# Optimization experiments

Measured on AMD Instinct MI355X. Metric: run time of the kernel, lower is better.

## Reference

```python
import jax, jax.numpy as jnp
import numpy as np

EPS = 1e-7
N_NODES = 100000

# --- Lorentz model (c = 1), working at the origin o = (1, 0, ..., 0) ---

def expmap0(v_spatial):
    """Exp map at origin: tangent spatial part [N, d] -> hyperboloid point [N, d+1]."""
    nrm = jnp.sqrt(jnp.maximum(jnp.sum(v_spatial * v_spatial, axis=-1, keepdims=True), EPS))
    x0 = jnp.cosh(nrm)
    xs = jnp.sinh(nrm) / nrm * v_spatial
    return jnp.concatenate([x0, xs], axis=-1)


def logmap0(x):
    """Log map at origin: point [N, d+1] -> tangent spatial part [N, d]."""
    x0 = jnp.maximum(x[..., :1], 1.0 + EPS)
    xs = x[..., 1:]
    nrm = jnp.sqrt(jnp.maximum(jnp.sum(xs * xs, axis=-1, keepdims=True), EPS))
    return jnp.arccosh(x0) / nrm * xs


def sigmoid_nonlin(x):
    # log map -> sigmoid in tangent space -> exp map (c_in = c_out = 1)
    return expmap0(jax.nn.sigmoid(logmap0(x)))


def hgcn_layer(x, edge_index, W, b):
    """HGCN conv: tangent-space linear + mean aggregation over edges + exp map."""
    t = logmap0(x)                      # [N, d_in]
    h = t @ W + b                       # [N, d_out]
    src, dst = edge_index[0], edge_index[1]
    msg = h[src]                        # [E, d_out] gather
    agg = jax.ops.segment_sum(msg, dst, num_segments=N_NODES)
    deg = jax.ops.segment_sum(jnp.ones((edge_index.shape[1],), h.dtype), dst,
                              num_segments=N_NODES)
    agg = agg / jnp.maximum(deg, 1.0)[:, None]
    return expmap0(agg)


def setup_inputs() -> dict:
    key = jax.random.key(0)
    ks = jax.random.split(key, 10)
    d_in, h1, h2, h_mlp, d_out = 64, 64, 64, 128, 40
    return {
        "features": jax.random.normal(ks[0], (N_NODES, d_in), jnp.float32),
        "edge_index": jax.random.randint(ks[1], (2, 1600000), 0, N_NODES, jnp.int64),
        "W1": jax.random.normal(ks[2], (d_in, h1), jnp.float32) * 0.05,
        "b1": jnp.zeros((h1,), jnp.float32),
        "W2": jax.random.normal(ks[3], (h1, h2), jnp.float32) * 0.05,
        "b2": jnp.zeros((h2,), jnp.float32),
        "W3": jax.random.normal(ks[4], (h2, h_mlp), jnp.float32) * 0.05,
        "b3": jnp.zeros((h_mlp,), jnp.float32),
        "W4": jax.random.normal(ks[5], (h_mlp, d_out), jnp.float32) * 0.05,
        "b4": jnp.zeros((d_out,), jnp.float32),
    }


def reference(features, edge_index, W1, b1, W2, b2, W3, b3, W4, b4):
    # lift Euclidean features to the hyperboloid (pad time coord, exp map)
    x = expmap0(features)                       # [N, d_in+1]
    x = hgcn_layer(x, edge_index, W1, b1)
    x = sigmoid_nonlin(x)
    x = hgcn_layer(x, edge_index, W2, b2)
    x = sigmoid_nonlin(x)
    t = logmap0(x)                              # [N, h2] (spatial part, drops time coord)
    # MLP head (dropout inactive at eval)
    h = jax.nn.relu(t @ W3 + b3)
    return h @ W4 + b4
```

## Files before the change

kernel.cpp:

```cpp
#include <hip/hip_runtime.h>


constexpr int CSHIFT = 8;
constexpr int CNODES = 1 << CSHIFT;
constexpr int EPB    = 4096;
constexpr int PTHR   = 512;
constexpr int EPT    = EPB / PTHR;
constexpr int CAP    = 6144;

constexpr int W1F_OFF = 0;
constexpr int W2F_OFF = 4096;
constexpr int W3F_OFF = 8192;
constexpr int W4F_OFF = 16384;
constexpr int WIMG_TOT = 22528;

typedef __attribute__((ext_vector_type(8))) short short8;
typedef __attribute__((ext_vector_type(4))) float floatx4;

__device__ __forceinline__ float sigmoidf(float x) {
    return 1.0f / (1.0f + __expf(-x));
}
__device__ __forceinline__ unsigned short f2bf(float f) {
    unsigned int u = __float_as_uint(f);
    u = (u + 0x7FFFu + ((u >> 16) & 1u)) >> 16;
    return (unsigned short)u;
}

__global__ __launch_bounds__(512) void part_prep_k(
    const int* __restrict__ src, const int* __restrict__ dst,
    int* __restrict__ ccur, int* __restrict__ arena, int E, int NBUCK, int gP,
    const float* __restrict__ feat, unsigned short* __restrict__ featbf,
    const float* __restrict__ W1, const float* __restrict__ W2,
    const float* __restrict__ W3, const float* __restrict__ W4,
    unsigned short* __restrict__ img, int n8)
{
    __shared__ int  hist[512];
    __shared__ int  exoff[512];
    __shared__ int  lcur[512];
    __shared__ int  gbase[512];
    __shared__ int  wsum[8];
    __shared__ int  stage[EPB];
    __shared__ unsigned short stageS[EPB];

    const int tid = threadIdx.x;

    if ((int)blockIdx.x >= gP) {
        int i = ((int)blockIdx.x - gP) * PTHR + tid;
        if (i < n8) {
            const float4* p = (const float4*)feat + (size_t)i * 2;
            float4 a = p[0], b = p[1];
            uint4 o;
            o.x = (unsigned)f2bf(a.x) | ((unsigned)f2bf(a.y) << 16);
            o.y = (unsigned)f2bf(a.z) | ((unsigned)f2bf(a.w) << 16);
            o.z = (unsigned)f2bf(b.x) | ((unsigned)f2bf(b.y) << 16);
            o.w = (unsigned)f2bf(b.z) | ((unsigned)f2bf(b.w) << 16);
            ((uint4*)featbf)[i] = o;
            return;
        }
        int t = i - n8;
        if (t >= WIMG_TOT) return;
        float v = 0.f;
        int s = t;
        if (s < W2F_OFF) {
            int j = s & 7, m = (s >> 3) & 15, q = (s >> 7) & 3, kk = (s >> 9) & 1, c = s >> 10;
            v = W1[(kk * 32 + q * 8 + j) * 64 + c * 16 + m];
        } else if (s < W3F_OFF) {
            s -= W2F_OFF;
            int j = s & 7, m = (s >> 3) & 15, q = (s >> 7) & 3, kk = (s >> 9) & 1, c = s >> 10;
            v = W2[(kk * 32 + q * 8 + j) * 64 + c * 16 + m];
        } else if (s < W4F_OFF) {
            s -= W3F_OFF;
            int j = s & 7, m = (s >> 3) & 15, q = (s >> 7) & 3, kk = (s >> 9) & 1, c = s >> 10;
            v = W3[(kk * 32 + q * 8 + j) * 128 + c * 16 + m];
        } else {
            s -= W4F_OFF;
            int j = s & 7, m = (s >> 3) & 15, q = (s >> 7) & 3, kk = (s >> 9) & 3, c = s >> 11;
            int n = c * 16 + m;
            if (n < 40) v = W4[(kk * 32 + q * 8 + j) * 40 + n];
        }
        img[t] = f2bf(v);
        return;
    }

    const int e0  = blockIdx.x * EPB;
    const int ec  = min(EPB, E - e0);
    const int lane = tid & 63, wid = tid >> 6;

    int pk[EPT], bk[EPT];
    hist[tid] = 0;
    __syncthreads();
    #pragma unroll
    for (int j = 0; j < EPT; j++) {
        int idx = tid + j * PTHR;
        if (idx < ec) {
            int s = src[e0 + idx];
            int d = dst[e0 + idx];
            bk[j] = d >> CSHIFT;
            pk[j] = s | ((d & (CNODES - 1)) << 17);
            atomicAdd(&hist[bk[j]], 1);
        } else bk[j] = -1;
    }
    __syncthreads();
    int h = hist[tid];
    int v = h;
    #pragma unroll
    for (int d = 1; d < 64; d <<= 1) {
        int t = __shfl_up(v, d);
        if (lane >= d) v += t;
    }
    if (lane == 63) wsum[wid] = v;
    __syncthreads();
    if (tid == 0) {
        int s = 0;
        #pragma unroll
        for (int k = 0; k < 8; k++) { int t = wsum[k]; wsum[k] = s; s += t; }
    }
    __syncthreads();
    {
        int ex = wsum[wid] + v - h;
        int gb = 0;
        if (tid < NBUCK && h > 0) gb = atomicAdd(ccur + tid, h);
        exoff[tid] = ex;
        lcur[tid]  = ex;
        gbase[tid] = gb;
    }
    __syncthreads();
    #pragma unroll
    for (int j = 0; j < EPT; j++) {
        if (bk[j] >= 0) {
            int l = atomicAdd(&lcur[bk[j]], 1);
            stage[l]  = pk[j];
            stageS[l] = (unsigned short)bk[j];
        }
    }
    __syncthreads();
    for (int i = tid; i < ec; i += PTHR) {
        int b = stageS[i];
        arena[(size_t)b * CAP + gbase[b] + (i - exoff[b])] = stage[i];
    }
}

__global__ __launch_bounds__(1024) void csr_fine(const int* __restrict__ arena,
                                                 const int* __restrict__ ccur,
                                                 int* __restrict__ off,
                                                 int* __restrict__ ssrc,
                                                 int N, int E, int NBUCK) {
    __shared__ int part[512];
    __shared__ int cnt[CNODES];
    __shared__ int cur[CNODES];
    __shared__ int wpre[8];
    __shared__ int wpre2[4];
    const int b = blockIdx.x;
    const int node0 = b << CSHIFT;
    const int tid = threadIdx.x;
    const int lane = tid & 63, wid = tid >> 6;

    int c0 = 0, v0 = 0;
    if (tid < 512) {
        c0 = (tid < NBUCK) ? ccur[tid] : 0;
        v0 = c0;
        #pragma unroll
        for (int d = 1; d < 64; d <<= 1) {
            int t = __shfl_up(v0, d);
            if (lane >= d) v0 += t;
        }
        if (lane == 63) wpre[wid] = v0;
    }
    __syncthreads();
    if (tid == 0) {
        int s = 0;
        #pragma unroll
        for (int k = 0; k < 8; k++) { int t = wpre[k]; wpre[k] = s; s += t; }
    }
    __syncthreads();
    if (tid < 512) part[tid] = wpre[wid] + v0;
    __syncthreads();
    const int cbeg = (b > 0) ? part[b - 1] : 0;
    const int ec   = min(ccur[b], CAP);
    if (b == 0 && tid == 0) off[N] = E;

    if (tid < CNODES) cnt[tid] = 0;
    __syncthreads();
    const int* pe = arena + (size_t)b * CAP;
    for (int i = tid; i < ec; i += 1024)
        atomicAdd(&cnt[(pe[i] >> 17) & (CNODES - 1)], 1);
    __syncthreads();

    int c = 0, v = 0;
    if (tid < CNODES) {
        c = cnt[tid];
        v = c;
        #pragma unroll
        for (int d = 1; d < 64; d <<= 1) {
            int t = __shfl_up(v, d);
            if (lane >= d) v += t;
        }
        if (lane == 63) wpre2[wid] = v;
    }
    __syncthreads();
    if (tid == 0) {
        int s = 0;
        #pragma unroll
        for (int k = 0; k < CNODES / 64; k++) { int t = wpre2[k]; wpre2[k] = s; s += t; }
    }
    __syncthreads();
    if (tid < CNODES) {
        int ex = wpre2[wid] + v - c;
        cur[tid] = ex;
        int node = node0 + tid;
        if (node < N) off[node] = cbeg + ex;
    }
    __syncthreads();
    for (int i = tid; i < ec; i += 1024) {
        int p = pe[i];
        int pos = cbeg + atomicAdd(&cur[(p >> 17) & (CNODES - 1)], 1);
        ssrc[pos] = p & 0x1FFFF;
    }
}

#define ACC8(v)                                    \
    acc[0] += __uint_as_float((v).x << 16);        \
    acc[1] += __uint_as_float((v).x & 0xFFFF0000u);\
    acc[2] += __uint_as_float((v).y << 16);        \
    acc[3] += __uint_as_float((v).y & 0xFFFF0000u);\
    acc[4] += __uint_as_float((v).z << 16);        \
    acc[5] += __uint_as_float((v).z & 0xFFFF0000u);\
    acc[6] += __uint_as_float((v).w << 16);        \
    acc[7] += __uint_as_float((v).w & 0xFFFF0000u);

__device__ __forceinline__ void gather_tile_wave(
    const unsigned short* __restrict__ h, const int* __restrict__ off,
    const int* __restrict__ ssrc, unsigned short* Agg, int rowB, int N,
    int w, int lane)
{
    #pragma unroll
    for (int pass = 0; pass < 2; pass++) {
        int rl = w * 16 + pass * 8 + (lane >> 3);
        int g  = rowB + rl;
        int q  = (lane & 7) * 8;
        uint4 p = make_uint4(0u, 0u, 0u, 0u);
        if (g < N) {
            int beg = off[g], end = off[g + 1];
            float acc[8] = {0.f, 0.f, 0.f, 0.f, 0.f, 0.f, 0.f, 0.f};
            int i = beg;
            for (; i + 8 <= end; i += 8) {
                uint4 v0 = *(const uint4*)(h + (size_t)ssrc[i]     * 64 + q);
                uint4 v1 = *(const uint4*)(h + (size_t)ssrc[i + 1] * 64 + q);
                uint4 v2 = *(const uint4*)(h + (size_t)ssrc[i + 2] * 64 + q);
                uint4 v3 = *(const uint4*)(h + (size_t)ssrc[i + 3] * 64 + q);
                uint4 v4 = *(const uint4*)(h + (size_t)ssrc[i + 4] * 64 + q);
                uint4 v5 = *(const uint4*)(h + (size_t)ssrc[i + 5] * 64 + q);
                uint4 v6 = *(const uint4*)(h + (size_t)ssrc[i + 6] * 64 + q);
                uint4 v7 = *(const uint4*)(h + (size_t)ssrc[i + 7] * 64 + q);
                ACC8(v0); ACC8(v1); ACC8(v2); ACC8(v3);
                ACC8(v4); ACC8(v5); ACC8(v6); ACC8(v7);
            }
            for (; i + 2 <= end; i += 2) {
                uint4 v0 = *(const uint4*)(h + (size_t)ssrc[i]     * 64 + q);
                uint4 v1 = *(const uint4*)(h + (size_t)ssrc[i + 1] * 64 + q);
                ACC8(v0); ACC8(v1);
            }
            for (; i < end; i++) {
                uint4 v = *(const uint4*)(h + (size_t)ssrc[i] * 64 + q);
                ACC8(v);
            }
            float inv = __builtin_amdgcn_rcpf((float)max(end - beg, 1));
            p.x = (unsigned)f2bf(acc[0]*inv) | ((unsigned)f2bf(acc[1]*inv) << 16);
            p.y = (unsigned)f2bf(acc[2]*inv) | ((unsigned)f2bf(acc[3]*inv) << 16);
            p.z = (unsigned)f2bf(acc[4]*inv) | ((unsigned)f2bf(acc[5]*inv) << 16);
            p.w = (unsigned)f2bf(acc[6]*inv) | ((unsigned)f2bf(acc[7]*inv) << 16);
        }
        *(uint4*)(Agg + rl * 72 + q) = p;
    }
}

__global__ __launch_bounds__(128) void aggemm1_k(
    const unsigned short* __restrict__ featbf, const int* __restrict__ off,
    const int* __restrict__ ssrc, const unsigned short* __restrict__ img,
    const float* __restrict__ bias, unsigned short* __restrict__ t1, int N)
{
    __shared__ alignas(16) unsigned short Agg[32 * 72];

    const int tid = threadIdx.x;
    const int rowB = blockIdx.x * 32;
    const int w = tid >> 6, lane = tid & 63;
    const int m = lane & 15, quad = lane >> 4;
    const int row0 = rowB + w * 16;

    gather_tile_wave(featbf, off, ssrc, Agg, rowB, N, w, lane);

    const short8* Wf = (const short8*)(img + W1F_OFF);
    floatx4 acc[4];
    #pragma unroll
    for (int c = 0; c < 4; c++) acc[c] = (floatx4){0.f, 0.f, 0.f, 0.f};
    #pragma unroll
    for (int kk = 0; kk < 2; kk++) {
        short8 a = *(const short8*)(Agg + (w * 16 + m) * 72 + kk * 32 + quad * 8);
        #pragma unroll
        for (int c = 0; c < 4; c++) {
            short8 b = Wf[((c * 2 + kk) * 4 + quad) * 16 + m];
            acc[c] = __builtin_amdgcn_mfma_f32_16x16x32_bf16(a, b, acc[c], 0, 0, 0);
        }
    }
    bool dzr[4];
    int rows[4];
    #pragma unroll
    for (int r = 0; r < 4; r++) {
        rows[r] = row0 + quad * 4 + r;
        dzr[r] = (rows[r] < N) ? (off[rows[r] + 1] == off[rows[r]]) : false;
    }
    #pragma unroll
    for (int c = 0; c < 4; c++) {
        int col = c * 16 + m;
        float bv = bias[col];
        #pragma unroll
        for (int r = 0; r < 4; r++) {
            if (rows[r] < N) {
                float v = dzr[r] ? 0.5f : sigmoidf(acc[c][r] + bv);
                t1[(size_t)rows[r] * 64 + col] = f2bf(v);
            }
        }
    }
}

__global__ __launch_bounds__(128) void aggep3_k(
    const unsigned short* __restrict__ t1, const int* __restrict__ off,
    const int* __restrict__ ssrc, const unsigned short* __restrict__ img,
    const float* __restrict__ b2, const float* __restrict__ b3,
    const float* __restrict__ b4, float* __restrict__ out, int N)
{
    __shared__ alignas(16) unsigned short SM[4608];
    unsigned short* T2  = SM;
    unsigned short* Agg = SM + 2304;
    unsigned short* H3h = SM + 2304;

    const int tid = threadIdx.x;
    const int rowB = blockIdx.x * 32;
    const int w = tid >> 6, lane = tid & 63;
    const int m = lane & 15, quad = lane >> 4;
    const int row0 = rowB + w * 16;

    gather_tile_wave(t1, off, ssrc, Agg, rowB, N, w, lane);

    {
        const short8* Wf = (const short8*)(img + W2F_OFF);
        floatx4 acc[4];
        #pragma unroll
        for (int c = 0; c < 4; c++) acc[c] = (floatx4){0.f, 0.f, 0.f, 0.f};
        #pragma unroll
        for (int kk = 0; kk < 2; kk++) {
            short8 a = *(const short8*)(Agg + (w * 16 + m) * 72 + kk * 32 + quad * 8);
            #pragma unroll
            for (int c = 0; c < 4; c++) {
                short8 b = Wf[((c * 2 + kk) * 4 + quad) * 16 + m];
                acc[c] = __builtin_amdgcn_mfma_f32_16x16x32_bf16(a, b, acc[c], 0, 0, 0);
            }
        }
        bool dzr[4];
        #pragma unroll
        for (int r = 0; r < 4; r++) {
            int row = row0 + quad * 4 + r;
            dzr[r] = (row < N) ? (off[row + 1] == off[row]) : false;
        }
        #pragma unroll
        for (int c = 0; c < 4; c++) {
            int col = c * 16 + m;
            float bv = b2[col];
            #pragma unroll
            for (int r = 0; r < 4; r++) {
                int rl = w * 16 + quad * 4 + r;
                float v = dzr[r] ? 0.5f : sigmoidf(acc[c][r] + bv);
                T2[rl * 72 + col] = f2bf(v);
            }
        }
    }

    floatx4 acc2[3];
    #pragma unroll
    for (int c = 0; c < 3; c++) acc2[c] = (floatx4){0.f, 0.f, 0.f, 0.f};
    const short8* Wf3 = (const short8*)(img + W3F_OFF);
    const short8* Wf4 = (const short8*)(img + W4F_OFF);

    #pragma unroll
    for (int half = 0; half < 2; half++) {
        floatx4 acc[4];
        #pragma unroll
        for (int c = 0; c < 4; c++) acc[c] = (floatx4){0.f, 0.f, 0.f, 0.f};
        #pragma unroll
        for (int kk = 0; kk < 2; kk++) {
            short8 a = *(const short8*)(T2 + (w * 16 + m) * 72 + kk * 32 + quad * 8);
            #pragma unroll
            for (int c = 0; c < 4; c++) {
                short8 b = Wf3[(((half * 4 + c) * 2 + kk) * 4 + quad) * 16 + m];
                acc[c] = __builtin_amdgcn_mfma_f32_16x16x32_bf16(a, b, acc[c], 0, 0, 0);
            }
        }
        #pragma unroll
        for (int c = 0; c < 4; c++) {
            int col = c * 16 + m;
            float bv = b3[half * 64 + col];
            #pragma unroll
            for (int r = 0; r < 4; r++) {
                int rl = w * 16 + quad * 4 + r;
                H3h[rl * 72 + col] = f2bf(fmaxf(acc[c][r] + bv, 0.f));
            }
        }
        #pragma unroll
        for (int kk2 = 0; kk2 < 2; kk2++) {
            short8 a = *(const short8*)(H3h + (w * 16 + m) * 72 + kk2 * 32 + quad * 8);
            #pragma unroll
            for (int c = 0; c < 3; c++) {
                short8 b = Wf4[((c * 4 + half * 2 + kk2) * 4 + quad) * 16 + m];
                acc2[c] = __builtin_amdgcn_mfma_f32_16x16x32_bf16(a, b, acc2[c], 0, 0, 0);
            }
        }
    }

    #pragma unroll
    for (int c = 0; c < 3; c++) {
        int col = c * 16 + m;
        if (col < 40) {
            float bv = b4[col];
            #pragma unroll
            for (int r = 0; r < 4; r++) {
                int row = row0 + quad * 4 + r;
                if (row < N) out[(size_t)row * 40 + col] = acc2[c][r] + bv;
            }
        }
    }
}

extern "C" void kernel_launch(void* const* d_in, const int* in_sizes, int n_in,
                              void* d_out, int out_size, void* d_ws, size_t ws_size,
                              hipStream_t stream)
{
    const float* feat = (const float*)d_in[0];
    const int*   eidx = (const int*)d_in[1];
    const float* W1 = (const float*)d_in[2];
    const float* b1 = (const float*)d_in[3];
    const float* W2 = (const float*)d_in[4];
    const float* b2 = (const float*)d_in[5];
    const float* W3 = (const float*)d_in[6];
    const float* b3 = (const float*)d_in[7];
    const float* W4 = (const float*)d_in[8];
    const float* b4 = (const float*)d_in[9];

    const int N = in_sizes[0] / 64;
    const int E = in_sizes[1] / 2;
    const int* src = eidx;
    const int* dst = eidx + E;

    const int NBUCK = (N + CNODES - 1) / CNODES;

    unsigned short* featbf = (unsigned short*)d_ws;
    unsigned short* t1     = featbf + (size_t)N * 64;
    unsigned short* img    = t1     + (size_t)N * 64;
    int*   off   = (int*)(img + WIMG_TOT);
    int*   ccur  = off + (N + 1);
    int*   ssrc  = ccur + NBUCK;
    int*   arena = ssrc + E;
    float* out   = (float*)d_out;

    hipMemsetAsync(ccur, 0, (size_t)NBUCK * sizeof(int), stream);

    const int gP  = (E + EPB - 1) / EPB;
    const int g32 = (N + 31) / 32;
    const int n8  = N * 64 / 8;
    const int gPC = (n8 + WIMG_TOT + PTHR - 1) / PTHR;

    part_prep_k<<<gP + gPC, dim3(PTHR), 0, stream>>>(src, dst, ccur, arena, E,
                                                     NBUCK, gP, feat, featbf,
                                                     W1, W2, W3, W4, img, n8);
    csr_fine<<<NBUCK, dim3(1024), 0, stream>>>(arena, ccur, off, ssrc, N, E, NBUCK);

    aggemm1_k<<<g32, dim3(128), 0, stream>>>(featbf, off, ssrc, img, b1, t1, N);
    aggep3_k<<<g32, dim3(128), 0, stream>>>(t1, off, ssrc, img, b2, b3, b4, out, N);
}
```

Before: 211.7 us.

## Sort CSR neighbors by source sub-range and enlarge gather blocks to 128 rows

The fine CSR build now buckets each destination node's edges into 8 sub-bins by source index high bits, so the neighbor lists are ordered by source region and the offset array becomes 8 entries per node. The intent is better cache locality for the feature gathers. The aggregation kernels also move from 32-row, 128-thread blocks to 128-row, 512-thread blocks with correspondingly larger shared memory. This costs an 8x larger offset array, more shared-memory atomics and scan work in csr_fine, and changes occupancy.

```diff
diff --git a/kernel.cpp b/kernel.cpp
--- a/kernel.cpp
+++ b/kernel.cpp
@@ -7,6 +7,8 @@
 constexpr int PTHR   = 512;
 constexpr int EPT    = EPB / PTHR;
 constexpr int CAP    = 6144;
+constexpr int SSH    = 14;
+constexpr int NBIN   = CNODES * 8;
 
 constexpr int W1F_OFF = 0;
 constexpr int W2F_OFF = 4096;
@@ -142,14 +144,14 @@
 
 __global__ __launch_bounds__(1024) void csr_fine(const int* __restrict__ arena,
                                                  const int* __restrict__ ccur,
-                                                 int* __restrict__ off,
+                                                 int* __restrict__ off2,
                                                  int* __restrict__ ssrc,
                                                  int N, int E, int NBUCK) {
     __shared__ int part[512];
-    __shared__ int cnt[CNODES];
-    __shared__ int cur[CNODES];
+    __shared__ int cnt[NBIN];
+    __shared__ int cur[NBIN];
     __shared__ int wpre[8];
-    __shared__ int wpre2[4];
+    __shared__ int wpre2[16];
     const int b = blockIdx.x;
     const int node0 = b << CSHIFT;
     const int tid = threadIdx.x;
@@ -177,43 +179,51 @@
     __syncthreads();
     const int cbeg = (b > 0) ? part[b - 1] : 0;
     const int ec   = min(ccur[b], CAP);
-    if (b == 0 && tid == 0) off[N] = E;
-
-    if (tid < CNODES) cnt[tid] = 0;
+    if (b == 0 && tid == 0) off2[8 * N] = E;
+
+    cnt[tid] = 0;
+    cnt[tid + 1024] = 0;
     __syncthreads();
     const int* pe = arena + (size_t)b * CAP;
-    for (int i = tid; i < ec; i += 1024)
-        atomicAdd(&cnt[(pe[i] >> 17) & (CNODES - 1)], 1);
-    __syncthreads();
-
-    int c = 0, v = 0;
-    if (tid < CNODES) {
-        c = cnt[tid];
-        v = c;
-        #pragma unroll
-        for (int d = 1; d < 64; d <<= 1) {
-            int t = __shfl_up(v, d);
-            if (lane >= d) v += t;
-        }
-        if (lane == 63) wpre2[wid] = v;
-    }
+    for (int i = tid; i < ec; i += 1024) {
+        int p = pe[i];
+        int key = (((p >> 17) & (CNODES - 1)) << 3) | ((p & 0x1FFFF) >> SSH);
+        atomicAdd(&cnt[key], 1);
+    }
+    __syncthreads();
+
+    const int t2 = tid * 2;
+    int s0 = cnt[t2], s1 = cnt[t2 + 1];
+    int tsum = s0 + s1;
+    int v = tsum;
+    #pragma unroll
+    for (int d = 1; d < 64; d <<= 1) {
+        int t = __shfl_up(v, d);
+        if (lane >= d) v += t;
+    }
+    if (lane == 63) wpre2[wid] = v;
     __syncthreads();
     if (tid == 0) {
         int s = 0;
         #pragma unroll
-        for (int k = 0; k < CNODES / 64; k++) { int t = wpre2[k]; wpre2[k] = s; s += t; }
-    }
-    __syncthreads();
-    if (tid < CNODES) {
-        int ex = wpre2[wid] + v - c;
-        cur[tid] = ex;
-        int node = node0 + tid;
-        if (node < N) off[node] = cbeg + ex;
+        for (int k = 0; k < 16; k++) { int t = wpre2[k]; wpre2[k] = s; s += t; }
+    }
+    __syncthreads();
+    const int ex0 = wpre2[wid] + v - tsum;
+    cur[t2]     = ex0;
+    cur[t2 + 1] = ex0 + s0;
+    {
+        int node = node0 + (t2 >> 3);
+        if (node < N) {
+            off2[node0 * 8 + t2]     = cbeg + ex0;
+            off2[node0 * 8 + t2 + 1] = cbeg + ex0 + s0;
+        }
     }
     __syncthreads();
     for (int i = tid; i < ec; i += 1024) {
         int p = pe[i];
-        int pos = cbeg + atomicAdd(&cur[(p >> 17) & (CNODES - 1)], 1);
+        int key = (((p >> 17) & (CNODES - 1)) << 3) | ((p & 0x1FFFF) >> SSH);
+        int pos = cbeg + atomicAdd(&cur[key], 1);
         ssrc[pos] = p & 0x1FFFF;
     }
 }
@@ -229,7 +239,7 @@
     acc[7] += __uint_as_float((v).w & 0xFFFF0000u);
 
 __device__ __forceinline__ void gather_tile_wave(
-    const unsigned short* __restrict__ h, const int* __restrict__ off,
+    const unsigned short* __restrict__ h, const int* __restrict__ off2,
     const int* __restrict__ ssrc, unsigned short* Agg, int rowB, int N,
     int w, int lane)
 {
@@ -240,7 +250,7 @@
         int q  = (lane & 7) * 8;
         uint4 p = make_uint4(0u, 0u, 0u, 0u);
         if (g < N) {
-            int beg = off[g], end = off[g + 1];
+            int beg = off2[g * 8], end = off2[g * 8 + 8];
             float acc[8] = {0.f, 0.f, 0.f, 0.f, 0.f, 0.f, 0.f, 0.f};
             int i = beg;
             for (; i + 8 <= end; i += 8) {
@@ -274,20 +284,20 @@
     }
 }
 
-__global__ __launch_bounds__(128) void aggemm1_k(
-    const unsigned short* __restrict__ featbf, const int* __restrict__ off,
+__global__ __launch_bounds__(512) void aggemm1_k(
+    const unsigned short* __restrict__ featbf, const int* __restrict__ off2,
     const int* __restrict__ ssrc, const unsigned short* __restrict__ img,
     const float* __restrict__ bias, unsigned short* __restrict__ t1, int N)
 {
-    __shared__ alignas(16) unsigned short Agg[32 * 72];
+    __shared__ alignas(16) unsigned short Agg[128 * 72];
 
     const int tid = threadIdx.x;
-    const int rowB = blockIdx.x * 32;
+    const int rowB = blockIdx.x * 128;
     const int w = tid >> 6, lane = tid & 63;
     const int m = lane & 15, quad = lane >> 4;
     const int row0 = rowB + w * 16;
 
-    gather_tile_wave(featbf, off, ssrc, Agg, rowB, N, w, lane);
+    gather_tile_wave(featbf, off2, ssrc, Agg, rowB, N, w, lane);
 
     const short8* Wf = (const short8*)(img + W1F_OFF);
     floatx4 acc[4];
@@ -307,7 +317,7 @@
     #pragma unroll
     for (int r = 0; r < 4; r++) {
         rows[r] = row0 + quad * 4 + r;
-        dzr[r] = (rows[r] < N) ? (off[rows[r] + 1] == off[rows[r]]) : false;
+        dzr[r] = (rows[r] < N) ? (off2[rows[r] * 8 + 8] == off2[rows[r] * 8]) : false;
     }
     #pragma unroll
     for (int c = 0; c < 4; c++) {
@@ -323,24 +333,24 @@
     }
 }
 
-__global__ __launch_bounds__(128) void aggep3_k(
-    const unsigned short* __restrict__ t1, const int* __restrict__ off,
+__global__ __launch_bounds__(512) void aggep3_k(
+    const unsigned short* __restrict__ t1, const int* __restrict__ off2,
     const int* __restrict__ ssrc, const unsigned short* __restrict__ img,
     const float* __restrict__ b2, const float* __restrict__ b3,
     const float* __restrict__ b4, float* __restrict__ out, int N)
 {
-    __shared__ alignas(16) unsigned short SM[4608];
+    __shared__ alignas(16) unsigned short SM[18432];
     unsigned short* T2  = SM;
-    unsigned short* Agg = SM + 2304;
-    unsigned short* H3h = SM + 2304;
+    unsigned short* Agg = SM + 9216;
+    unsigned short* H3h = SM + 9216;
 
     const int tid = threadIdx.x;
-    const int rowB = blockIdx.x * 32;
+    const int rowB = blockIdx.x * 128;
     const int w = tid >> 6, lane = tid & 63;
     const int m = lane & 15, quad = lane >> 4;
     const int row0 = rowB + w * 16;
 
-    gather_tile_wave(t1, off, ssrc, Agg, rowB, N, w, lane);
+    gather_tile_wave(t1, off2, ssrc, Agg, rowB, N, w, lane);
 
     {
         const short8* Wf = (const short8*)(img + W2F_OFF);
@@ -360,7 +370,7 @@
         #pragma unroll
         for (int r = 0; r < 4; r++) {
             int row = row0 + quad * 4 + r;
-            dzr[r] = (row < N) ? (off[row + 1] == off[row]) : false;
+            dzr[r] = (row < N) ? (off2[row * 8 + 8] == off2[row * 8]) : false;
         }
         #pragma unroll
         for (int c = 0; c < 4; c++) {
@@ -455,24 +465,24 @@
     unsigned short* featbf = (unsigned short*)d_ws;
     unsigned short* t1     = featbf + (size_t)N * 64;
     unsigned short* img    = t1     + (size_t)N * 64;
-    int*   off   = (int*)(img + WIMG_TOT);
-    int*   ccur  = off + (N + 1);
+    int*   off2  = (int*)(img + WIMG_TOT);
+    int*   ccur  = off2 + ((size_t)8 * N + 1);
     int*   ssrc  = ccur + NBUCK;
     int*   arena = ssrc + E;
     float* out   = (float*)d_out;
 
     hipMemsetAsync(ccur, 0, (size_t)NBUCK * sizeof(int), stream);
 
-    const int gP  = (E + EPB - 1) / EPB;
-    const int g32 = (N + 31) / 32;
-    const int n8  = N * 64 / 8;
-    const int gPC = (n8 + WIMG_TOT + PTHR - 1) / PTHR;
+    const int gP   = (E + EPB - 1) / EPB;
+    const int g128 = (N + 127) / 128;
+    const int n8   = N * 64 / 8;
+    const int gPC  = (n8 + WIMG_TOT + PTHR - 1) / PTHR;
 
     part_prep_k<<<gP + gPC, dim3(PTHR), 0, stream>>>(src, dst, ccur, arena, E,
                                                      NBUCK, gP, feat, featbf,
                                                      W1, W2, W3, W4, img, n8);
-    csr_fine<<<NBUCK, dim3(1024), 0, stream>>>(arena, ccur, off, ssrc, N, E, NBUCK);
-
-    aggemm1_k<<<g32, dim3(128), 0, stream>>>(featbf, off, ssrc, img, b1, t1, N);
-    aggep3_k<<<g32, dim3(128), 0, stream>>>(t1, off, ssrc, img, b2, b3, b4, out, N);
-}
+    csr_fine<<<NBUCK, dim3(1024), 0, stream>>>(arena, ccur, off2, ssrc, N, E, NBUCK);
+
+    aggemm1_k<<<g128, dim3(512), 0, stream>>>(featbf, off2, ssrc, img, b1, t1, N);
+    aggep3_k<<<g128, dim3(512), 0, stream>>>(t1, off2, ssrc, img, b2, b3, b4, out, N);
+}
```

Measured after the change: 216.7 us. 1.02x slower.

## Merge partition, prep and CSR build into one cooperative kernel with grid syncs

Applied to the files above, without the earlier changes.

Replaces the memset, the partition/prep kernel and the CSR fine-sort kernel with one cooperative kernel that zeroes the bucket counters, partitions edges, converts features and weights, then builds the CSR after grid-wide barriers. The goal is to remove two launches and the memset plus their inter-kernel gaps. In exchange, feature conversion becomes a grid-stride loop over fewer blocks, CSR blocks now run with 512 threads instead of 1024, and grid.sync adds barrier cost. The cooperative launch also requires every block to be co-resident.

```diff
diff --git a/kernel.cpp b/kernel.cpp
--- a/kernel.cpp
+++ b/kernel.cpp
@@ -1,4 +1,7 @@
 #include <hip/hip_runtime.h>
+#include <hip/hip_cooperative_groups.h>
+
+namespace cg = cooperative_groups;
 
 
 constexpr int CSHIFT = 8;
@@ -26,14 +29,18 @@
     return (unsigned short)u;
 }
 
-__global__ __launch_bounds__(512) void part_prep_k(
+__global__ __launch_bounds__(PTHR) void prep_all_k(
     const int* __restrict__ src, const int* __restrict__ dst,
-    int* __restrict__ ccur, int* __restrict__ arena, int E, int NBUCK, int gP,
+    int* __restrict__ ccur, int* __restrict__ arena,
+    int* __restrict__ off, int* __restrict__ ssrc,
+    int E, int N, int NBUCK, int gP,
     const float* __restrict__ feat, unsigned short* __restrict__ featbf,
     const float* __restrict__ W1, const float* __restrict__ W2,
     const float* __restrict__ W3, const float* __restrict__ W4,
     unsigned short* __restrict__ img, int n8)
 {
+    cg::grid_group grid = cg::this_grid();
+
     __shared__ int  hist[512];
     __shared__ int  exoff[512];
     __shared__ int  lcur[512];
@@ -41,180 +48,177 @@
     __shared__ int  wsum[8];
     __shared__ int  stage[EPB];
     __shared__ unsigned short stageS[EPB];
+    __shared__ int  cnt[CNODES];
+    __shared__ int  cur[CNODES];
+    __shared__ int  wpre2[4];
+    __shared__ int  cbeg_s;
 
     const int tid = threadIdx.x;
-
-    if ((int)blockIdx.x >= gP) {
-        int i = ((int)blockIdx.x - gP) * PTHR + tid;
-        if (i < n8) {
-            const float4* p = (const float4*)feat + (size_t)i * 2;
-            float4 a = p[0], b = p[1];
-            uint4 o;
-            o.x = (unsigned)f2bf(a.x) | ((unsigned)f2bf(a.y) << 16);
-            o.y = (unsigned)f2bf(a.z) | ((unsigned)f2bf(a.w) << 16);
-            o.z = (unsigned)f2bf(b.x) | ((unsigned)f2bf(b.y) << 16);
-            o.w = (unsigned)f2bf(b.z) | ((unsigned)f2bf(b.w) << 16);
-            ((uint4*)featbf)[i] = o;
-            return;
-        }
-        int t = i - n8;
-        if (t >= WIMG_TOT) return;
-        float v = 0.f;
-        int s = t;
-        if (s < W2F_OFF) {
-            int j = s & 7, m = (s >> 3) & 15, q = (s >> 7) & 3, kk = (s >> 9) & 1, c = s >> 10;
-            v = W1[(kk * 32 + q * 8 + j) * 64 + c * 16 + m];
-        } else if (s < W3F_OFF) {
-            s -= W2F_OFF;
-            int j = s & 7, m = (s >> 3) & 15, q = (s >> 7) & 3, kk = (s >> 9) & 1, c = s >> 10;
-            v = W2[(kk * 32 + q * 8 + j) * 64 + c * 16 + m];
-        } else if (s < W4F_OFF) {
-            s -= W3F_OFF;
-            int j = s & 7, m = (s >> 3) & 15, q = (s >> 7) & 3, kk = (s >> 9) & 1, c = s >> 10;
-            v = W3[(kk * 32 + q * 8 + j) * 128 + c * 16 + m];
-        } else {
-            s -= W4F_OFF;
-            int j = s & 7, m = (s >> 3) & 15, q = (s >> 7) & 3, kk = (s >> 9) & 3, c = s >> 11;
-            int n = c * 16 + m;
-            if (n < 40) v = W4[(kk * 32 + q * 8 + j) * 40 + n];
-        }
-        img[t] = f2bf(v);
-        return;
-    }
-
-    const int e0  = blockIdx.x * EPB;
-    const int ec  = min(EPB, E - e0);
+    const int bid = blockIdx.x;
     const int lane = tid & 63, wid = tid >> 6;
 
-    int pk[EPT], bk[EPT];
-    hist[tid] = 0;
-    __syncthreads();
-    #pragma unroll
-    for (int j = 0; j < EPT; j++) {
-        int idx = tid + j * PTHR;
-        if (idx < ec) {
-            int s = src[e0 + idx];
-            int d = dst[e0 + idx];
-            bk[j] = d >> CSHIFT;
-            pk[j] = s | ((d & (CNODES - 1)) << 17);
-            atomicAdd(&hist[bk[j]], 1);
-        } else bk[j] = -1;
-    }
-    __syncthreads();
-    int h = hist[tid];
-    int v = h;
-    #pragma unroll
-    for (int d = 1; d < 64; d <<= 1) {
-        int t = __shfl_up(v, d);
-        if (lane >= d) v += t;
-    }
-    if (lane == 63) wsum[wid] = v;
-    __syncthreads();
-    if (tid == 0) {
-        int s = 0;
-        #pragma unroll
-        for (int k = 0; k < 8; k++) { int t = wsum[k]; wsum[k] = s; s += t; }
-    }
-    __syncthreads();
+    if (bid == 0 && tid < NBUCK) ccur[tid] = 0;
+    __threadfence();
+    grid.sync();
+
+    if (bid < gP) {
+        const int e0 = bid * EPB;
+        const int ec = min(EPB, E - e0);
+
+        int pk[EPT], bk[EPT];
+        hist[tid] = 0;
+        __syncthreads();
+        #pragma unroll
+        for (int j = 0; j < EPT; j++) {
+            int idx = tid + j * PTHR;
+            if (idx < ec) {
+                int s = src[e0 + idx];
+                int d = dst[e0 + idx];
+                bk[j] = d >> CSHIFT;
+                pk[j] = s | ((d & (CNODES - 1)) << 17);
+                atomicAdd(&hist[bk[j]], 1);
+            } else bk[j] = -1;
+        }
+        __syncthreads();
+        int h = hist[tid];
+        int v = h;
+        #pragma unroll
+        for (int d = 1; d < 64; d <<= 1) {
+            int t = __shfl_up(v, d);
+            if (lane >= d) v += t;
+        }
+        if (lane == 63) wsum[wid] = v;
+        __syncthreads();
+        if (tid == 0) {
+            int s = 0;
+            #pragma unroll
+            for (int k = 0; k < 8; k++) { int t = wsum[k]; wsum[k] = s; s += t; }
+        }
+        __syncthreads();
+        {
+            int ex = wsum[wid] + v - h;
+            int gb = 0;
+            if (tid < NBUCK && h > 0) gb = atomicAdd(ccur + tid, h);
+            exoff[tid] = ex;
+            lcur[tid]  = ex;
+            gbase[tid] = gb;
+        }
+        __syncthreads();
+        #pragma unroll
+        for (int j = 0; j < EPT; j++) {
+            if (bk[j] >= 0) {
+                int l = atomicAdd(&lcur[bk[j]], 1);
+                stage[l]  = pk[j];
+                stageS[l] = (unsigned short)bk[j];
+            }
+        }
+        __syncthreads();
+        for (int i = tid; i < ec; i += PTHR) {
+            int b = stageS[i];
+            arena[(size_t)b * CAP + gbase[b] + (i - exoff[b])] = stage[i];
+        }
+    }
+
     {
-        int ex = wsum[wid] + v - h;
-        int gb = 0;
-        if (tid < NBUCK && h > 0) gb = atomicAdd(ccur + tid, h);
-        exoff[tid] = ex;
-        lcur[tid]  = ex;
-        gbase[tid] = gb;
-    }
-    __syncthreads();
-    #pragma unroll
-    for (int j = 0; j < EPT; j++) {
-        if (bk[j] >= 0) {
-            int l = atomicAdd(&lcur[bk[j]], 1);
-            stage[l]  = pk[j];
-            stageS[l] = (unsigned short)bk[j];
-        }
-    }
-    __syncthreads();
-    for (int i = tid; i < ec; i += PTHR) {
-        int b = stageS[i];
-        arena[(size_t)b * CAP + gbase[b] + (i - exoff[b])] = stage[i];
-    }
-}
-
-__global__ __launch_bounds__(1024) void csr_fine(const int* __restrict__ arena,
-                                                 const int* __restrict__ ccur,
-                                                 int* __restrict__ off,
-                                                 int* __restrict__ ssrc,
-                                                 int N, int E, int NBUCK) {
-    __shared__ int part[512];
-    __shared__ int cnt[CNODES];
-    __shared__ int cur[CNODES];
-    __shared__ int wpre[8];
-    __shared__ int wpre2[4];
-    const int b = blockIdx.x;
-    const int node0 = b << CSHIFT;
-    const int tid = threadIdx.x;
-    const int lane = tid & 63, wid = tid >> 6;
-
-    int c0 = 0, v0 = 0;
-    if (tid < 512) {
-        c0 = (tid < NBUCK) ? ccur[tid] : 0;
-        v0 = c0;
+        const int nW = n8 + WIMG_TOT;
+        for (int i = bid * PTHR + tid; i < nW; i += gridDim.x * PTHR) {
+            if (i < n8) {
+                const float4* p = (const float4*)feat + (size_t)i * 2;
+                float4 a = p[0], b = p[1];
+                uint4 o;
+                o.x = (unsigned)f2bf(a.x) | ((unsigned)f2bf(a.y) << 16);
+                o.y = (unsigned)f2bf(a.z) | ((unsigned)f2bf(a.w) << 16);
+                o.z = (unsigned)f2bf(b.x) | ((unsigned)f2bf(b.y) << 16);
+                o.w = (unsigned)f2bf(b.z) | ((unsigned)f2bf(b.w) << 16);
+                ((uint4*)featbf)[i] = o;
+                continue;
+            }
+            int t = i - n8;
+            float v = 0.f;
+            int s = t;
+            if (s < W2F_OFF) {
+                int j = s & 7, m = (s >> 3) & 15, q = (s >> 7) & 3, kk = (s >> 9) & 1, c = s >> 10;
+                v = W1[(kk * 32 + q * 8 + j) * 64 + c * 16 + m];
+            } else if (s < W3F_OFF) {
+                s -= W2F_OFF;
+                int j = s & 7, m = (s >> 3) & 15, q = (s >> 7) & 3, kk = (s >> 9) & 1, c = s >> 10;
+                v = W2[(kk * 32 + q * 8 + j) * 64 + c * 16 + m];
+            } else if (s < W4F_OFF) {
+                s -= W3F_OFF;
+                int j = s & 7, m = (s >> 3) & 15, q = (s >> 7) & 3, kk = (s >> 9) & 1, c = s >> 10;
+                v = W3[(kk * 32 + q * 8 + j) * 128 + c * 16 + m];
+            } else {
+                s -= W4F_OFF;
+                int j = s & 7, m = (s >> 3) & 15, q = (s >> 7) & 3, kk = (s >> 9) & 3, c = s >> 11;
+                int n = c * 16 + m;
+                if (n < 40) v = W4[(kk * 32 + q * 8 + j) * 40 + n];
+            }
+            img[t] = f2bf(v);
+        }
+    }
+    __threadfence();
+    grid.sync();
+
+    if (bid < NBUCK) {
+        int c0 = (tid < NBUCK) ? ccur[tid] : 0;
+        int v0 = c0;
         #pragma unroll
         for (int d = 1; d < 64; d <<= 1) {
             int t = __shfl_up(v0, d);
             if (lane >= d) v0 += t;
         }
-        if (lane == 63) wpre[wid] = v0;
-    }
-    __syncthreads();
-    if (tid == 0) {
-        int s = 0;
-        #pragma unroll
-        for (int k = 0; k < 8; k++) { int t = wpre[k]; wpre[k] = s; s += t; }
-    }
-    __syncthreads();
-    if (tid < 512) part[tid] = wpre[wid] + v0;
-    __syncthreads();
-    const int cbeg = (b > 0) ? part[b - 1] : 0;
-    const int ec   = min(ccur[b], CAP);
-    if (b == 0 && tid == 0) off[N] = E;
-
-    if (tid < CNODES) cnt[tid] = 0;
-    __syncthreads();
-    const int* pe = arena + (size_t)b * CAP;
-    for (int i = tid; i < ec; i += 1024)
-        atomicAdd(&cnt[(pe[i] >> 17) & (CNODES - 1)], 1);
-    __syncthreads();
-
-    int c = 0, v = 0;
-    if (tid < CNODES) {
-        c = cnt[tid];
-        v = c;
-        #pragma unroll
-        for (int d = 1; d < 64; d <<= 1) {
-            int t = __shfl_up(v, d);
-            if (lane >= d) v += t;
-        }
-        if (lane == 63) wpre2[wid] = v;
-    }
-    __syncthreads();
-    if (tid == 0) {
-        int s = 0;
-        #pragma unroll
-        for (int k = 0; k < CNODES / 64; k++) { int t = wpre2[k]; wpre2[k] = s; s += t; }
-    }
-    __syncthreads();
-    if (tid < CNODES) {
-        int ex = wpre2[wid] + v - c;
-        cur[tid] = ex;
-        int node = node0 + tid;
-        if (node < N) off[node] = cbeg + ex;
-    }
-    __syncthreads();
-    for (int i = tid; i < ec; i += 1024) {
-        int p = pe[i];
-        int pos = cbeg + atomicAdd(&cur[(p >> 17) & (CNODES - 1)], 1);
-        ssrc[pos] = p & 0x1FFFF;
+        if (lane == 63) wsum[wid] = v0;
+        __syncthreads();
+        if (tid == 0) {
+            int s = 0;
+            #pragma unroll
+            for (int k = 0; k < 8; k++) { int t = wsum[k]; wsum[k] = s; s += t; }
+        }
+        __syncthreads();
+        if (tid == bid) cbeg_s = wsum[wid] + v0 - c0;
+        if (bid == 0 && tid == 0) off[N] = E;
+        __syncthreads();
+        const int cbeg = cbeg_s;
+        const int ec   = min(ccur[bid], CAP);
+        const int node0 = bid << CSHIFT;
+
+        if (tid < CNODES) cnt[tid] = 0;
+        __syncthreads();
+        const int* pe = arena + (size_t)bid * CAP;
+        for (int i = tid; i < ec; i += PTHR)
+            atomicAdd(&cnt[(pe[i] >> 17) & (CNODES - 1)], 1);
+        __syncthreads();
+
+        int c = 0, v = 0;
+        if (tid < CNODES) {
+            c = cnt[tid];
+            v = c;
+            #pragma unroll
+            for (int d = 1; d < 64; d <<= 1) {
+                int t = __shfl_up(v, d);
+                if (lane >= d) v += t;
+            }
+            if (lane == 63) wpre2[wid] = v;
+        }
+        __syncthreads();
+        if (tid == 0) {
+            int s = 0;
+            #pragma unroll
+            for (int k = 0; k < CNODES / 64; k++) { int t = wpre2[k]; wpre2[k] = s; s += t; }
+        }
+        __syncthreads();
+        if (tid < CNODES) {
+            int ex = wpre2[wid] + v - c;
+            cur[tid] = ex;
+            int node = node0 + tid;
+            if (node < N) off[node] = cbeg + ex;
+        }
+        __syncthreads();
+        for (int i = tid; i < ec; i += PTHR) {
+            int p = pe[i];
+            int pos = cbeg + atomicAdd(&cur[(p >> 17) & (CNODES - 1)], 1);
+            ssrc[pos] = p & 0x1FFFF;
+        }
     }
 }
 
@@ -461,17 +465,23 @@
     int*   arena = ssrc + E;
     float* out   = (float*)d_out;
 
-    hipMemsetAsync(ccur, 0, (size_t)NBUCK * sizeof(int), stream);
-
     const int gP  = (E + EPB - 1) / EPB;
+    const int n8  = N * 64 / 8;
     const int g32 = (N + 31) / 32;
-    const int n8  = N * 64 / 8;
-    const int gPC = (n8 + WIMG_TOT + PTHR - 1) / PTHR;
-
-    part_prep_k<<<gP + gPC, dim3(PTHR), 0, stream>>>(src, dst, ccur, arena, E,
-                                                     NBUCK, gP, feat, featbf,
-                                                     W1, W2, W3, W4, img, n8);
-    csr_fine<<<NBUCK, dim3(1024), 0, stream>>>(arena, ccur, off, ssrc, N, E, NBUCK);
+    const int G   = (gP > NBUCK) ? gP : NBUCK;
+
+    {
+        int E_ = E, N_ = N, NBUCK_ = NBUCK, gP_ = gP, n8_ = n8;
+        void* args[] = {
+            (void*)&src, (void*)&dst, (void*)&ccur, (void*)&arena,
+            (void*)&off, (void*)&ssrc, (void*)&E_, (void*)&N_, (void*)&NBUCK_,
+            (void*)&gP_, (void*)&feat, (void*)&featbf,
+            (void*)&W1, (void*)&W2, (void*)&W3, (void*)&W4,
+            (void*)&img, (void*)&n8_
+        };
+        hipLaunchCooperativeKernel((const void*)prep_all_k, dim3(G), dim3(PTHR),
+                                   args, 0, stream);
+    }
 
     aggemm1_k<<<g32, dim3(128), 0, stream>>>(featbf, off, ssrc, img, b1, t1, N);
     aggep3_k<<<g32, dim3(128), 0, stream>>>(t1, off, ssrc, img, b2, b3, b4, out, N);
```

Result: slower. 432.6 us (+104.3%).

## Fuse CSR bucket build with first-layer gather+GEMM into one kernel

Applied to the files above, without the earlier changes.

Merges the per-bucket CSR construction kernel with the first aggregation/MFMA kernel. Each 512-thread block now builds the CSR segment for its 256-node bucket, then immediately gathers and runs the matmul and sigmoid for those rows, taking degrees and offsets from shared memory. This removes one kernel launch and the global reads of the offset array. In exchange the layer-1 gather runs on far fewer, larger blocks (one per bucket instead of one per 32 rows), which lowers parallelism and the ability to hide gather latency.

```diff
diff --git a/kernel.cpp b/kernel.cpp
--- a/kernel.cpp
+++ b/kernel.cpp
@@ -140,84 +140,6 @@
     }
 }
 
-__global__ __launch_bounds__(1024) void csr_fine(const int* __restrict__ arena,
-                                                 const int* __restrict__ ccur,
-                                                 int* __restrict__ off,
-                                                 int* __restrict__ ssrc,
-                                                 int N, int E, int NBUCK) {
-    __shared__ int part[512];
-    __shared__ int cnt[CNODES];
-    __shared__ int cur[CNODES];
-    __shared__ int wpre[8];
-    __shared__ int wpre2[4];
-    const int b = blockIdx.x;
-    const int node0 = b << CSHIFT;
-    const int tid = threadIdx.x;
-    const int lane = tid & 63, wid = tid >> 6;
-
-    int c0 = 0, v0 = 0;
-    if (tid < 512) {
-        c0 = (tid < NBUCK) ? ccur[tid] : 0;
-        v0 = c0;
-        #pragma unroll
-        for (int d = 1; d < 64; d <<= 1) {
-            int t = __shfl_up(v0, d);
-            if (lane >= d) v0 += t;
-        }
-        if (lane == 63) wpre[wid] = v0;
-    }
-    __syncthreads();
-    if (tid == 0) {
-        int s = 0;
-        #pragma unroll
-        for (int k = 0; k < 8; k++) { int t = wpre[k]; wpre[k] = s; s += t; }
-    }
-    __syncthreads();
-    if (tid < 512) part[tid] = wpre[wid] + v0;
-    __syncthreads();
-    const int cbeg = (b > 0) ? part[b - 1] : 0;
-    const int ec   = min(ccur[b], CAP);
-    if (b == 0 && tid == 0) off[N] = E;
-
-    if (tid < CNODES) cnt[tid] = 0;
-    __syncthreads();
-    const int* pe = arena + (size_t)b * CAP;
-    for (int i = tid; i < ec; i += 1024)
-        atomicAdd(&cnt[(pe[i] >> 17) & (CNODES - 1)], 1);
-    __syncthreads();
-
-    int c = 0, v = 0;
-    if (tid < CNODES) {
-        c = cnt[tid];
-        v = c;
-        #pragma unroll
-        for (int d = 1; d < 64; d <<= 1) {
-            int t = __shfl_up(v, d);
-            if (lane >= d) v += t;
-        }
-        if (lane == 63) wpre2[wid] = v;
-    }
-    __syncthreads();
-    if (tid == 0) {
-        int s = 0;
-        #pragma unroll
-        for (int k = 0; k < CNODES / 64; k++) { int t = wpre2[k]; wpre2[k] = s; s += t; }
-    }
-    __syncthreads();
-    if (tid < CNODES) {
-        int ex = wpre2[wid] + v - c;
-        cur[tid] = ex;
-        int node = node0 + tid;
-        if (node < N) off[node] = cbeg + ex;
-    }
-    __syncthreads();
-    for (int i = tid; i < ec; i += 1024) {
-        int p = pe[i];
-        int pos = cbeg + atomicAdd(&cur[(p >> 17) & (CNODES - 1)], 1);
-        ssrc[pos] = p & 0x1FFFF;
-    }
-}
-
 #define ACC8(v)                                    \
     acc[0] += __uint_as_float((v).x << 16);        \
     acc[1] += __uint_as_float((v).x & 0xFFFF0000u);\
@@ -228,6 +150,179 @@
     acc[6] += __uint_as_float((v).w << 16);        \
     acc[7] += __uint_as_float((v).w & 0xFFFF0000u);
 
+__device__ __forceinline__ uint4 gather_row(
+    const unsigned short* __restrict__ h, const int* __restrict__ ssrc,
+    int beg, int end, int q)
+{
+    float acc[8] = {0.f, 0.f, 0.f, 0.f, 0.f, 0.f, 0.f, 0.f};
+    int i = beg;
+    for (; i + 8 <= end; i += 8) {
+        uint4 v0 = *(const uint4*)(h + (size_t)ssrc[i]     * 64 + q);
+        uint4 v1 = *(const uint4*)(h + (size_t)ssrc[i + 1] * 64 + q);
+        uint4 v2 = *(const uint4*)(h + (size_t)ssrc[i + 2] * 64 + q);
+        uint4 v3 = *(const uint4*)(h + (size_t)ssrc[i + 3] * 64 + q);
+        uint4 v4 = *(const uint4*)(h + (size_t)ssrc[i + 4] * 64 + q);
+        uint4 v5 = *(const uint4*)(h + (size_t)ssrc[i + 5] * 64 + q);
+        uint4 v6 = *(const uint4*)(h + (size_t)ssrc[i + 6] * 64 + q);
+        uint4 v7 = *(const uint4*)(h + (size_t)ssrc[i + 7] * 64 + q);
+        ACC8(v0); ACC8(v1); ACC8(v2); ACC8(v3);
+        ACC8(v4); ACC8(v5); ACC8(v6); ACC8(v7);
+    }
+    for (; i + 2 <= end; i += 2) {
+        uint4 v0 = *(const uint4*)(h + (size_t)ssrc[i]     * 64 + q);
+        uint4 v1 = *(const uint4*)(h + (size_t)ssrc[i + 1] * 64 + q);
+        ACC8(v0); ACC8(v1);
+    }
+    for (; i < end; i++) {
+        uint4 v = *(const uint4*)(h + (size_t)ssrc[i] * 64 + q);
+        ACC8(v);
+    }
+    float inv = __builtin_amdgcn_rcpf((float)max(end - beg, 1));
+    uint4 p;
+    p.x = (unsigned)f2bf(acc[0]*inv) | ((unsigned)f2bf(acc[1]*inv) << 16);
+    p.y = (unsigned)f2bf(acc[2]*inv) | ((unsigned)f2bf(acc[3]*inv) << 16);
+    p.z = (unsigned)f2bf(acc[4]*inv) | ((unsigned)f2bf(acc[5]*inv) << 16);
+    p.w = (unsigned)f2bf(acc[6]*inv) | ((unsigned)f2bf(acc[7]*inv) << 16);
+    return p;
+}
+
+__global__ __launch_bounds__(512) void aggemm1s_k(
+    const unsigned short* __restrict__ featbf, const int* __restrict__ ccur,
+    const int* __restrict__ arena, int* __restrict__ off,
+    int* __restrict__ ssrc, const unsigned short* __restrict__ img,
+    const float* __restrict__ bias, unsigned short* __restrict__ t1,
+    int N, int E, int NBUCK)
+{
+    __shared__ int part[512];
+    __shared__ int wsum[8];
+    __shared__ int cnt[CNODES];
+    __shared__ int beg2[CNODES];
+    __shared__ int cur[CNODES];
+    __shared__ int wpre2[4];
+    __shared__ alignas(16) unsigned short Agg[CNODES * 72];
+
+    const int tid = threadIdx.x;
+    const int bid = blockIdx.x;
+    const int lane = tid & 63, wid = tid >> 6;
+    const int rowB = bid << CSHIFT;
+
+    int c0 = (tid < NBUCK) ? ccur[tid] : 0;
+    int v0 = c0;
+    #pragma unroll
+    for (int d = 1; d < 64; d <<= 1) {
+        int t = __shfl_up(v0, d);
+        if (lane >= d) v0 += t;
+    }
+    if (lane == 63) wsum[wid] = v0;
+    __syncthreads();
+    if (tid == 0) {
+        int s = 0;
+        #pragma unroll
+        for (int k = 0; k < 8; k++) { int t = wsum[k]; wsum[k] = s; s += t; }
+    }
+    __syncthreads();
+    part[tid] = wsum[wid] + v0;
+    __syncthreads();
+    const int cbeg = (bid > 0) ? part[bid - 1] : 0;
+    const int ec   = min(ccur[bid], CAP);
+    if (bid == 0 && tid == 0) off[N] = E;
+
+    if (tid < CNODES) cnt[tid] = 0;
+    __syncthreads();
+    const int* pe = arena + (size_t)bid * CAP;
+    for (int i = tid; i < ec; i += 512)
+        atomicAdd(&cnt[(pe[i] >> 17) & (CNODES - 1)], 1);
+    __syncthreads();
+
+    int c = 0, v = 0;
+    if (tid < CNODES) {
+        c = cnt[tid];
+        v = c;
+        #pragma unroll
+        for (int d = 1; d < 64; d <<= 1) {
+            int t = __shfl_up(v, d);
+            if (lane >= d) v += t;
+        }
+        if (lane == 63) wpre2[wid] = v;
+    }
+    __syncthreads();
+    if (tid == 0) {
+        int s = 0;
+        #pragma unroll
+        for (int k = 0; k < CNODES / 64; k++) { int t = wpre2[k]; wpre2[k] = s; s += t; }
+    }
+    __syncthreads();
+    if (tid < CNODES) {
+        int ex = wpre2[wid] + v - c;
+        beg2[tid] = ex;
+        cur[tid]  = ex;
+        int node = rowB + tid;
+        if (node < N) off[node] = cbeg + ex;
+    }
+    __syncthreads();
+
+    for (int i = tid; i < ec; i += 512) {
+        int p = pe[i];
+        int pos = cbeg + atomicAdd(&cur[(p >> 17) & (CNODES - 1)], 1);
+        ssrc[pos] = p & 0x1FFFF;
+    }
+    __syncthreads();
+
+    const int w = wid;
+    const int q = (lane & 7) * 8;
+    #pragma unroll
+    for (int pass = 0; pass < 4; pass++) {
+        int rl = w * 32 + pass * 8 + (lane >> 3);
+        int g  = rowB + rl;
+        uint4 p = make_uint4(0u, 0u, 0u, 0u);
+        if (g < N) {
+            int beg = cbeg + beg2[rl];
+            int end = beg + cnt[rl];
+            p = gather_row(featbf, ssrc, beg, end, q);
+        }
+        *(uint4*)(Agg + rl * 72 + q) = p;
+    }
+
+    const int m = lane & 15, quad = lane >> 4;
+    const short8* Wf = (const short8*)(img + W1F_OFF);
+    #pragma unroll
+    for (int sub = 0; sub < 2; sub++) {
+        const int r0l = w * 32 + sub * 16;
+        floatx4 acc[4];
+        #pragma unroll
+        for (int cc = 0; cc < 4; cc++) acc[cc] = (floatx4){0.f, 0.f, 0.f, 0.f};
+        #pragma unroll
+        for (int kk = 0; kk < 2; kk++) {
+            short8 a = *(const short8*)(Agg + (r0l + m) * 72 + kk * 32 + quad * 8);
+            #pragma unroll
+            for (int cc = 0; cc < 4; cc++) {
+                short8 b = Wf[((cc * 2 + kk) * 4 + quad) * 16 + m];
+                acc[cc] = __builtin_amdgcn_mfma_f32_16x16x32_bf16(a, b, acc[cc], 0, 0, 0);
+            }
+        }
+        bool dzr[4];
+        int rows[4];
+        #pragma unroll
+        for (int r = 0; r < 4; r++) {
+            int rl = r0l + quad * 4 + r;
+            rows[r] = rowB + rl;
+            dzr[r] = (cnt[rl] == 0);
+        }
+        #pragma unroll
+        for (int cc = 0; cc < 4; cc++) {
+            int col = cc * 16 + m;
+            float bv = bias[col];
+            #pragma unroll
+            for (int r = 0; r < 4; r++) {
+                if (rows[r] < N) {
+                    float vv = dzr[r] ? 0.5f : sigmoidf(acc[cc][r] + bv);
+                    t1[(size_t)rows[r] * 64 + col] = f2bf(vv);
+                }
+            }
+        }
+    }
+}
+
 __device__ __forceinline__ void gather_tile_wave(
     const unsigned short* __restrict__ h, const int* __restrict__ off,
     const int* __restrict__ ssrc, unsigned short* Agg, int rowB, int N,
@@ -240,86 +335,9 @@
         int q  = (lane & 7) * 8;
         uint4 p = make_uint4(0u, 0u, 0u, 0u);
         if (g < N) {
-            int beg = off[g], end = off[g + 1];
-            float acc[8] = {0.f, 0.f, 0.f, 0.f, 0.f, 0.f, 0.f, 0.f};
-            int i = beg;
-            for (; i + 8 <= end; i += 8) {
-                uint4 v0 = *(const uint4*)(h + (size_t)ssrc[i]     * 64 + q);
-                uint4 v1 = *(const uint4*)(h + (size_t)ssrc[i + 1] * 64 + q);
-                uint4 v2 = *(const uint4*)(h + (size_t)ssrc[i + 2] * 64 + q);
-                uint4 v3 = *(const uint4*)(h + (size_t)ssrc[i + 3] * 64 + q);
-                uint4 v4 = *(const uint4*)(h + (size_t)ssrc[i + 4] * 64 + q);
-                uint4 v5 = *(const uint4*)(h + (size_t)ssrc[i + 5] * 64 + q);
-                uint4 v6 = *(const uint4*)(h + (size_t)ssrc[i + 6] * 64 + q);
-                uint4 v7 = *(const uint4*)(h + (size_t)ssrc[i + 7] * 64 + q);
-                ACC8(v0); ACC8(v1); ACC8(v2); ACC8(v3);
-                ACC8(v4); ACC8(v5); ACC8(v6); ACC8(v7);
-            }
-            for (; i + 2 <= end; i += 2) {
-                uint4 v0 = *(const uint4*)(h + (size_t)ssrc[i]     * 64 + q);
-                uint4 v1 = *(const uint4*)(h + (size_t)ssrc[i + 1] * 64 + q);
-                ACC8(v0); ACC8(v1);
-            }
-            for (; i < end; i++) {
-                uint4 v = *(const uint4*)(h + (size_t)ssrc[i] * 64 + q);
-                ACC8(v);
-            }
-            float inv = __builtin_amdgcn_rcpf((float)max(end - beg, 1));
-            p.x = (unsigned)f2bf(acc[0]*inv) | ((unsigned)f2bf(acc[1]*inv) << 16);
-            p.y = (unsigned)f2bf(acc[2]*inv) | ((unsigned)f2bf(acc[3]*inv) << 16);
-            p.z = (unsigned)f2bf(acc[4]*inv) | ((unsigned)f2bf(acc[5]*inv) << 16);
-            p.w = (unsigned)f2bf(acc[6]*inv) | ((unsigned)f2bf(acc[7]*inv) << 16);
+            p = gather_row(h, ssrc, off[g], off[g + 1], q);
         }
         *(uint4*)(Agg + rl * 72 + q) = p;
-    }
-}
-
-__global__ __launch_bounds__(128) void aggemm1_k(
-    const unsigned short* __restrict__ featbf, const int* __restrict__ off,
-    const int* __restrict__ ssrc, const unsigned short* __restrict__ img,
-    const float* __restrict__ bias, unsigned short* __restrict__ t1, int N)
-{
-    __shared__ alignas(16) unsigned short Agg[32 * 72];
-
-    const int tid = threadIdx.x;
-    const int rowB = blockIdx.x * 32;
-    const int w = tid >> 6, lane = tid & 63;
-    const int m = lane & 15, quad = lane >> 4;
-    const int row0 = rowB + w * 16;
-
-    gather_tile_wave(featbf, off, ssrc, Agg, rowB, N, w, lane);
-
-    const short8* Wf = (const short8*)(img + W1F_OFF);
-    floatx4 acc[4];
-    #pragma unroll
-    for (int c = 0; c < 4; c++) acc[c] = (floatx4){0.f, 0.f, 0.f, 0.f};
-    #pragma unroll
-    for (int kk = 0; kk < 2; kk++) {
-        short8 a = *(const short8*)(Agg + (w * 16 + m) * 72 + kk * 32 + quad * 8);
-        #pragma unroll
-        for (int c = 0; c < 4; c++) {
-            short8 b = Wf[((c * 2 + kk) * 4 + quad) * 16 + m];
-            acc[c] = __builtin_amdgcn_mfma_f32_16x16x32_bf16(a, b, acc[c], 0, 0, 0);
-        }
-    }
-    bool dzr[4];
-    int rows[4];
-    #pragma unroll
-    for (int r = 0; r < 4; r++) {
-        rows[r] = row0 + quad * 4 + r;
-        dzr[r] = (rows[r] < N) ? (off[rows[r] + 1] == off[rows[r]]) : false;
-    }
-    #pragma unroll
-    for (int c = 0; c < 4; c++) {
-        int col = c * 16 + m;
-        float bv = bias[col];
-        #pragma unroll
-        for (int r = 0; r < 4; r++) {
-            if (rows[r] < N) {
-                float v = dzr[r] ? 0.5f : sigmoidf(acc[c][r] + bv);
-                t1[(size_t)rows[r] * 64 + col] = f2bf(v);
-            }
-        }
     }
 }
 
@@ -464,15 +482,16 @@
     hipMemsetAsync(ccur, 0, (size_t)NBUCK * sizeof(int), stream);
 
     const int gP  = (E + EPB - 1) / EPB;
+    const int n8  = N * 64 / 8;
     const int g32 = (N + 31) / 32;
-    const int n8  = N * 64 / 8;
     const int gPC = (n8 + WIMG_TOT + PTHR - 1) / PTHR;
 
     part_prep_k<<<gP + gPC, dim3(PTHR), 0, stream>>>(src, dst, ccur, arena, E,
                                                      NBUCK, gP, feat, featbf,
                                                      W1, W2, W3, W4, img, n8);
-    csr_fine<<<NBUCK, dim3(1024), 0, stream>>>(arena, ccur, off, ssrc, N, E, NBUCK);
-
-    aggemm1_k<<<g32, dim3(128), 0, stream>>>(featbf, off, ssrc, img, b1, t1, N);
+
+    aggemm1s_k<<<NBUCK, dim3(512), 0, stream>>>(featbf, ccur, arena, off, ssrc,
+                                                img, b1, t1, N, E, NBUCK);
+
     aggep3_k<<<g32, dim3(128), 0, stream>>>(t1, off, ssrc, img, b2, b3, b4, out, N);
 }
```

Measured after the change: 206.9 us. 2.3% less time.
